# Kernel optimization log

Hardware: AMD Instinct MI355X
Metric: run time of the kernel (lower is better)

Reference implementation:

```python
import jax, jax.numpy as jnp
import numpy as np

T, B, F, H = 128, 64, 75, 512
J = F  # attention dim == number of input features (joints)


def _lstm_dir(x, h0, c0, Wih, Whh, bih, bhh, reverse):
    # x: (T,B,Fin). Precompute input projection once (big GEMM), scan the recurrence.
    xw = jnp.einsum('tbf,gf->tbg', x, Wih) + bih + bhh  # (T,B,4H)

    def step(carry, xt):
        h, c = carry
        g = xt + h @ Whh.T  # (B,4H), PyTorch gate order i,f,g,o
        i, f, gg, o = jnp.split(g, 4, axis=-1)
        c = jax.nn.sigmoid(f) * c + jax.nn.sigmoid(i) * jnp.tanh(gg)
        h = jax.nn.sigmoid(o) * jnp.tanh(c)
        return (h, c), h

    (hT, cT), ys = jax.lax.scan(step, (h0, c0), xw, reverse=reverse)
    return ys, hT


def _bilstm(x, h0, c0, Wih, Whh, bih, bhh):
    # params have leading direction axis of size 2
    yf, hf = _lstm_dir(x, h0[0], c0[0], Wih[0], Whh[0], bih[0], bhh[0], False)
    yb, hb = _lstm_dir(x, h0[1], c0[1], Wih[1], Whh[1], bih[1], bhh[1], True)
    return jnp.concatenate([yf, yb], axis=-1), jnp.stack([hf, hb])


def setup_inputs() -> dict:
    key = jax.random.key(0)
    ks = iter(jax.random.split(key, 40))

    def p(*shape):
        return (jax.random.normal(next(ks), shape, dtype=jnp.float32) * 0.05)

    inp = {
        'x': jax.random.normal(next(ks), (T, B, F), dtype=jnp.float32),
        'h0': jnp.zeros((6, B, H), jnp.float32),
        'c0': jnp.zeros((6, B, H), jnp.float32),
        # salstm: 1-layer bidirectional, input F
        'sa_Wih': p(2, 4 * H, F), 'sa_Whh': p(2, 4 * H, H),
        'sa_bih': p(2, 4 * H), 'sa_bhh': p(2, 4 * H),
        # mainlstm layer 0 (input F)
        'm0_Wih': p(2, 4 * H, F), 'm0_Whh': p(2, 4 * H, H),
        'm0_bih': p(2, 4 * H), 'm0_bhh': p(2, 4 * H),
        # mainlstm layers 1,2 (input 2H), stacked on leading layer axis
        'mL_Wih': p(2, 2, 4 * H, 2 * H), 'mL_Whh': p(2, 2, 4 * H, H),
        'mL_bih': p(2, 2, 4 * H), 'mL_bhh': p(2, 2, 4 * H),
        'safc1_W': p(H, H), 'safc1_b': p(H),
        'safc2_W': p(J, H), 'safc2_b': p(J),
        'fc1_W': p(H, 2 * H), 'fc1_b': p(H),
    }
    return inp


def reference(x, h0, c0, sa_Wih, sa_Whh, sa_bih, sa_bhh,
              m0_Wih, m0_Whh, m0_bih, m0_bhh,
              mL_Wih, mL_Whh, mL_bih, mL_bhh,
              safc1_W, safc1_b, safc2_W, safc2_b, fc1_W, fc1_b):
    # spatial-attention LSTM
    sa_out, sa_hn = _bilstm(x, h0[:2], c0[:2], sa_Wih, sa_Whh, sa_bih, sa_bhh)  # sa_hn (2,B,H)
    e = jnp.exp(jnp.tanh(sa_hn @ safc1_W.T + safc1_b) @ safc2_W.T + safc2_b)  # (2,B,J)
    alpha = e / e.sum(axis=(0, 2), keepdims=True)  # per-batch normalization
    # replace all weights >= 0.1 with their selected mean (per batch element)
    mask = alpha >= 0.1
    cnt = mask.sum(axis=(0, 2), keepdims=True)
    sel_mean = (alpha * mask).sum(axis=(0, 2), keepdims=True) / jnp.maximum(cnt, 1)
    alpha = jnp.where(mask, sel_mean, alpha)
    alpha_b = alpha.mean(axis=0)  # (B,J) -- reconcile direction axis for broadcast

    xw = x * alpha_b[None]  # (T,B,F)

    # 3-layer bidirectional main LSTM
    y, _ = _bilstm(xw, h0[0:2], c0[0:2], m0_Wih, m0_Whh, m0_bih, m0_bhh)
    for l in range(2):
        y, _ = _bilstm(y, h0[2 + 2 * l:4 + 2 * l], c0[2 + 2 * l:4 + 2 * l],
                       mL_Wih[l], mL_Whh[l], mL_bih[l], mL_bhh[l])
    out = y @ fc1_W.T + fc1_b  # (T,B,H)
    return out
```

## Files before the change

### kernel.cpp

```cpp
#include <hip/hip_runtime.h>
#include <cstddef>

#define T_  128
#define B_  64
#define F_  75
#define H_  512
#define G4_ 2048
#define TB_ (T_ * B_)
#define KP_ 128

typedef __bf16 bf16x8 __attribute__((ext_vector_type(8)));
typedef float  f32x4  __attribute__((ext_vector_type(4)));
typedef unsigned long long u64;
typedef unsigned long long __attribute__((may_alias)) u64a;

__device__ __forceinline__ short f2b(float x) {
    union { float f; unsigned u; } v; v.f = x;
    return (short)((v.u + 0x7fffu + ((v.u >> 16) & 1u)) >> 16);
}
__device__ __forceinline__ float b2f(short s) {
    union { float f; unsigned u; } v; v.u = ((unsigned)(unsigned short)s) << 16;
    return v.f;
}
__device__ __forceinline__ void gload16(const void* g, void* l) {
    __builtin_amdgcn_global_load_lds(
        (const __attribute__((address_space(1))) void*)g,
        (__attribute__((address_space(3))) void*)l, 16, 0, 0);
}
__device__ __forceinline__ float fsig(float x) {
    return __builtin_amdgcn_rcpf(1.f + __expf(-x));
}
__device__ __forceinline__ float ftanh(float x) {
    return 1.f - 2.f * __builtin_amdgcn_rcpf(1.f + __expf(2.f * x));
}

__global__ __launch_bounds__(256) void gemm_bf16(
    const short* __restrict__ A, const short* __restrict__ Bm,
    float* __restrict__ C, float* __restrict__ P, int M, int N, int K,
    const float* __restrict__ bias1, const float* __restrict__ bias2)
{
    __shared__ short As[4096];
    __shared__ short Bs[4096];
    const int tid = threadIdx.x;
    const int m_base = blockIdx.y * 128;
    const int n_base = blockIdx.x * 128;
    const int w = tid >> 6, lane = tid & 63;
    const int wm = (w >> 1) * 64, wn = (w & 1) * 64;
    const int lm = lane & 15, q = lane >> 4;

    f32x4 acc[4][4];
#pragma unroll
    for (int i = 0; i < 4; i++)
#pragma unroll
        for (int j = 0; j < 4; j++)
#pragma unroll
            for (int r = 0; r < 4; r++) acc[i][j][r] = 0.f;

    const int s0 = tid, s1 = tid + 256;
    const int r0 = s0 & 127, c0 = s0 >> 7;
    const int r1 = s1 & 127, c1 = s1 >> 7;

    for (int k0 = 0; k0 < K; k0 += 32) {
        __syncthreads();
        gload16(A + (size_t)(m_base + r0) * K + k0 + c0 * 8, &As[s0 * 8]);
        gload16(A + (size_t)(m_base + r1) * K + k0 + c1 * 8, &As[s1 * 8]);
        gload16(Bm + (size_t)(n_base + r0) * K + k0 + c0 * 8, &Bs[s0 * 8]);
        gload16(Bm + (size_t)(n_base + r1) * K + k0 + c1 * 8, &Bs[s1 * 8]);
        __syncthreads();
        bf16x8 af[4], bfv[4];
#pragma unroll
        for (int i = 0; i < 4; i++) {
            af[i]  = *(const bf16x8*)&As[((q * 128) + wm + i * 16 + lm) * 8];
            bfv[i] = *(const bf16x8*)&Bs[((q * 128) + wn + i * 16 + lm) * 8];
        }
#pragma unroll
        for (int i = 0; i < 4; i++)
#pragma unroll
            for (int j = 0; j < 4; j++)
                acc[i][j] = __builtin_amdgcn_mfma_f32_16x16x32_bf16(
                    af[i], bfv[j], acc[i][j], 0, 0, 0);
    }

#pragma unroll
    for (int i = 0; i < 4; i++) {
#pragma unroll
        for (int j = 0; j < 4; j++) {
            const int gm0 = m_base + wm + i * 16 + q * 4;
            const int gn = n_base + wn + j * 16 + lm;
            float bb = (bias1 ? bias1[gn] : 0.f) + (bias2 ? bias2[gn] : 0.f);
            if (P) {
                const int g = gn >> 9, u = gn & 511;
                const int ub = u >> 4, lmu = u & 15;
#pragma unroll
                for (int r = 0; r < 4; r++) {
                    const int gm = gm0 + r;
                    const int t = gm >> 6, b = gm & 63;
                    const int tidS = (b >> 4) * 64 + ((b >> 2) & 3) * 16 + lmu;
                    size_t idx = ((((size_t)t * 32 + ub) * 4 + (b & 3)) * 256 + tidS) * 4 + g;
                    P[idx] = acc[i][j][r] + bb;
                }
            } else {
#pragma unroll
                for (int r = 0; r < 4; r++)
                    C[(size_t)(gm0 + r) * N + gn] = acc[i][j][r] + bb;
            }
        }
    }
}

__global__ __launch_bounds__(256) void pack_whh(
    const float* __restrict__ W, short* __restrict__ Wpk)
{
    int i = blockIdx.x * 256 + threadIdx.x;
    if (i >= 2 * G4_ * H_) return;
    int e = i & 7, lane = (i >> 3) & 63, it = (i >> 9) & 15;
    int g = (i >> 13) & 3, ub = (i >> 15) & 31, dir = (i >> 20) & 1;
    int lm = lane & 15, qq = lane >> 4;
    float v = W[((size_t)dir * G4_ + g * H_ + ub * 16 + lm) * H_
                + it * 32 + qq * 8 + e];
    Wpk[i] = f2b(v);
}

__global__ __launch_bounds__(256) void init_phase(
    const float* __restrict__ h0s, short* __restrict__ Ht,
    unsigned* __restrict__ bar, int zero_bar)
{
    int i = blockIdx.x * 256 + threadIdx.x;
    if (i < 2 * B_ * H_) Ht[i] = f2b(h0s[i]);
    if (zero_bar && i < 64) bar[i] = 0;
}

__global__ __launch_bounds__(256) void ht_to_f32(
    const short* __restrict__ Ht0, float* __restrict__ out)
{
    int i = blockIdx.x * 256 + threadIdx.x;
    if (i < 2 * B_ * H_) out[i] = b2f(Ht0[i]);
}

__global__ __launch_bounds__(256, 1) void lstm_phase(
    const float* __restrict__ XW,
    const short* __restrict__ Wpk,
    short* __restrict__ Ht,
    const float* __restrict__ c0p,
    short* __restrict__ Y,
    unsigned* __restrict__ bar, int phase)
{
    __shared__ short Ws[32768];
    __shared__ short Tb[64 * 24];
    __shared__ unsigned arrv;
    const int dir = blockIdx.y, ub = blockIdx.x, u0 = ub * 16;
    const int tid = threadIdx.x, w = tid >> 6, lane = tid & 63;
    const int lm = lane & 15, q = lane >> 4;

    if (tid == 0) arrv = 0;

    const short* wsrc = Wpk + (size_t)(dir * 32 + ub) * 32768;
#pragma unroll
    for (int p = 0; p < 16; p++)
        gload16(wsrc + (tid + 256 * p) * 8, &Ws[(tid + 256 * p) * 8]);

    const int b0 = w * 16 + q * 4;
    const int u = u0 + lm;
    unsigned* slots = bar + dir * 32;

    float c[4];
    f32x4 xw[4];
#pragma unroll
    for (int r = 0; r < 4; r++)
        c[r] = c0p[(size_t)dir * B_ * H_ + (size_t)(b0 + r) * H_ + u];
    {
        const int t0 = dir ? (T_ - 1) : 0;
        const float* xp = XW + ((size_t)dir * T_ + t0) * (B_ * G4_) + (size_t)ub * 4096;
#pragma unroll
        for (int r = 0; r < 4; r++)
            xw[r] = *(const f32x4*)(xp + r * 1024 + tid * 4);
    }
    __syncthreads();

    for (int s = 0; s < T_; s++) {
        const int t = dir ? (T_ - 1 - s) : s;
        const short* Hc = Ht + ((size_t)((s & 1) * 2 + dir) << 15);

        u64 hq[32];
        const short* hrow = Hc + (w * 16 + lm) * 512 + q * 8;
#pragma unroll
        for (int it = 0; it < 16; it++) {
            const u64* hp = (const u64*)(hrow + it * 32);
            hq[2 * it]     = __hip_atomic_load((u64*)hp,     __ATOMIC_RELAXED, __HIP_MEMORY_SCOPE_AGENT);
            hq[2 * it + 1] = __hip_atomic_load((u64*)hp + 1, __ATOMIC_RELAXED, __HIP_MEMORY_SCOPE_AGENT);
        }

        f32x4 acc[4];
#pragma unroll
        for (int g = 0; g < 4; g++)
#pragma unroll
            for (int r = 0; r < 4; r++) acc[g][r] = 0.f;

#pragma unroll
        for (int it = 0; it < 16; it++) {
            union { u64 q2[2]; bf16x8 v; } ua;
            ua.q2[0] = hq[2 * it]; ua.q2[1] = hq[2 * it + 1];
#pragma unroll
            for (int g = 0; g < 4; g++) {
                bf16x8 bv = *(const bf16x8*)&Ws[((g * 16 + it) * 64 + lane) * 8];
                acc[g] = __builtin_amdgcn_mfma_f32_16x16x32_bf16(ua.v, bv, acc[g], 0, 0, 0);
            }
        }

#pragma unroll
        for (int r = 0; r < 4; r++) {
            float gi = acc[0][r] + xw[r][0];
            float gf = acc[1][r] + xw[r][1];
            float gg = acc[2][r] + xw[r][2];
            float go = acc[3][r] + xw[r][3];
            float cc = fsig(gf) * c[r] + fsig(gi) * ftanh(gg);
            c[r] = cc;
            Tb[(b0 + r) * 24 + lm] = f2b(fsig(go) * ftanh(cc));
        }
        __asm__ volatile("" ::: "memory");

        const int b = tid >> 2, qd = tid & 3;
        u64 v0 = *(const u64a*)&Tb[b * 24 + qd * 4];
        {
            short* Hn = Ht + ((size_t)(((s + 1) & 1) * 2 + dir) << 15);
            __hip_atomic_store((u64*)(Hn + b * 512 + u0 + qd * 4), v0,
                               __ATOMIC_RELAXED, __HIP_MEMORY_SCOPE_AGENT);
        }
        __asm__ volatile("s_waitcnt vmcnt(0)" ::: "memory");
        if (lane == 0)
            __hip_atomic_fetch_add(&arrv, 1u, __ATOMIC_RELAXED,
                                   __HIP_MEMORY_SCOPE_WORKGROUP);

        const unsigned tgt = (unsigned)(phase * T_ + s + 1);
        if (w == 0) {
            const unsigned a4 = 4u * (unsigned)(s + 1);
            while (__hip_atomic_load(&arrv, __ATOMIC_RELAXED,
                                     __HIP_MEMORY_SCOPE_WORKGROUP) < a4) {}
            if (lane == 0)
                __hip_atomic_store(&slots[ub], tgt,
                                   __ATOMIC_RELAXED, __HIP_MEMORY_SCOPE_AGENT);
        }

        if (Y)
            *(u64a*)(Y + ((size_t)t * B_ + b) * (2 * H_) + dir * H_ + u0 + qd * 4) = v0;
        if (s < T_ - 1) {
            const int tn = dir ? (T_ - 2 - s) : (s + 1);
            const float* xp = XW + ((size_t)dir * T_ + tn) * (B_ * G4_) + (size_t)ub * 4096;
#pragma unroll
            for (int r = 0; r < 4; r++)
                xw[r] = *(const f32x4*)(xp + r * 1024 + tid * 4);

            if (w == 0) {
                unsigned v;
                for (;;) {
                    v = (lane < 32)
                        ? __hip_atomic_load(&slots[lane], __ATOMIC_RELAXED, __HIP_MEMORY_SCOPE_AGENT)
                        : tgt;
                    if (__all(v >= tgt)) break;
                    __builtin_amdgcn_s_sleep(1);
                }
            }
            __syncthreads();
        }
    }
}

__global__ __launch_bounds__(256) void gemm_bt(
    const float* __restrict__ A, const float* __restrict__ Bm,
    float* __restrict__ C, int M, int N, int K,
    const float* __restrict__ bias1, int act)
{
    __shared__ float As[16][68];
    __shared__ float Bs[16][68];
    const int tid = threadIdx.x;
    const int m_base = blockIdx.y * 64;
    const int n_base = blockIdx.x * 64;
    const int tm = tid >> 4, tn = tid & 15;
    float acc[4][4] = {};

    for (int k0 = 0; k0 < K; k0 += 16) {
#pragma unroll
        for (int i = 0; i < 4; i++) {
            int idx = tid * 4 + i;
            int r = idx >> 4, kk = idx & 15;
            int gm = m_base + r, gk = k0 + kk;
            As[kk][r] = (gm < M && gk < K) ? A[(size_t)gm * K + gk] : 0.f;
            int gn = n_base + r;
            Bs[kk][r] = (gn < N && gk < K) ? Bm[(size_t)gn * K + gk] : 0.f;
        }
        __syncthreads();
#pragma unroll
        for (int kk = 0; kk < 16; kk++) {
            float4 av = *(const float4*)&As[kk][tm * 4];
            float4 bv = *(const float4*)&Bs[kk][tn * 4];
            float a[4] = {av.x, av.y, av.z, av.w};
            float b[4] = {bv.x, bv.y, bv.z, bv.w};
#pragma unroll
            for (int i = 0; i < 4; i++)
#pragma unroll
                for (int j = 0; j < 4; j++)
                    acc[i][j] = fmaf(a[i], b[j], acc[i][j]);
        }
        __syncthreads();
    }
#pragma unroll
    for (int i = 0; i < 4; i++) {
        int gm = m_base + tm * 4 + i;
        if (gm >= M) continue;
#pragma unroll
        for (int j = 0; j < 4; j++) {
            int gn = n_base + tn * 4 + j;
            if (gn >= N) continue;
            float v = acc[i][j];
            if (bias1) v += bias1[gn];
            if (act == 1) v = tanhf(v);
            else if (act == 2) v = expf(v);
            C[(size_t)gm * N + gn] = v;
        }
    }
}

__global__ __launch_bounds__(256) void conv_f2b(
    const float* __restrict__ src, short* __restrict__ dst, int n)
{
    int i = blockIdx.x * 256 + threadIdx.x;
    if (i < n) dst[i] = f2b(src[i]);
}
__global__ __launch_bounds__(256) void conv_f2b_pad(
    const float* __restrict__ src, short* __restrict__ dst,
    int rows, int kin, int kp)
{
    int i = blockIdx.x * 256 + threadIdx.x;
    if (i < rows * kp) {
        int r = i / kp, k = i % kp;
        dst[i] = (k < kin) ? f2b(src[(size_t)r * kin + k]) : (short)0;
    }
}

__global__ __launch_bounds__(256) void attn_alpha(
    const float* __restrict__ E, float* __restrict__ AB)
{
    const int b = blockIdx.x, tid = threadIdx.x;
    __shared__ float red[256];
    __shared__ float adj[152];
    float v = 0.f;
    if (tid < 150) {
        int d = tid / F_, j = tid % F_;
        v = E[((size_t)d * B_ + b) * F_ + j];
    }
    red[tid] = v; __syncthreads();
    for (int s2 = 128; s2 > 0; s2 >>= 1) {
        if (tid < s2) red[tid] += red[tid + s2];
        __syncthreads();
    }
    float total = red[0]; __syncthreads();
    float alpha = v / total;
    float m = (tid < 150 && alpha >= 0.1f) ? 1.f : 0.f;
    red[tid] = m; __syncthreads();
    for (int s2 = 128; s2 > 0; s2 >>= 1) {
        if (tid < s2) red[tid] += red[tid + s2];
        __syncthreads();
    }
    float cnt = red[0]; __syncthreads();
    red[tid] = m * alpha; __syncthreads();
    for (int s2 = 128; s2 > 0; s2 >>= 1) {
        if (tid < s2) red[tid] += red[tid + s2];
        __syncthreads();
    }
    float selsum = red[0]; __syncthreads();
    float selmean = selsum / fmaxf(cnt, 1.f);
    if (tid < 150) adj[tid] = (m > 0.f) ? selmean : alpha;
    __syncthreads();
    if (tid < F_) AB[(size_t)b * F_ + tid] = 0.5f * (adj[tid] + adj[F_ + tid]);
}

__global__ __launch_bounds__(256) void scale_xb(
    const float* __restrict__ x, const float* __restrict__ AB,
    short* __restrict__ xb)
{
    int i = blockIdx.x * 256 + threadIdx.x;
    if (i < TB_ * KP_) {
        int r = i >> 7, k = i & 127;
        if (k < F_) {
            int b = r % B_;
            xb[i] = f2b(x[(size_t)r * F_ + k] * AB[(size_t)b * F_ + k]);
        } else xb[i] = 0;
    }
}

extern "C" void kernel_launch(void* const* d_in, const int* in_sizes, int n_in,
                              void* d_out, int out_size, void* d_ws, size_t ws_size,
                              hipStream_t stream)
{
    (void)in_sizes; (void)n_in; (void)out_size; (void)ws_size;
    const float* x       = (const float*)d_in[0];
    const float* h0      = (const float*)d_in[1];
    const float* c0      = (const float*)d_in[2];
    const float* sa_Wih  = (const float*)d_in[3];
    const float* sa_Whh  = (const float*)d_in[4];
    const float* sa_bih  = (const float*)d_in[5];
    const float* sa_bhh  = (const float*)d_in[6];
    const float* m0_Wih  = (const float*)d_in[7];
    const float* m0_Whh  = (const float*)d_in[8];
    const float* m0_bih  = (const float*)d_in[9];
    const float* m0_bhh  = (const float*)d_in[10];
    const float* mL_Wih  = (const float*)d_in[11];
    const float* mL_Whh  = (const float*)d_in[12];
    const float* mL_bih  = (const float*)d_in[13];
    const float* mL_bhh  = (const float*)d_in[14];
    const float* safc1_W = (const float*)d_in[15];
    const float* safc1_b = (const float*)d_in[16];
    const float* safc2_W = (const float*)d_in[17];
    const float* safc2_b = (const float*)d_in[18];
    const float* fc1_W   = (const float*)d_in[19];
    const float* fc1_b   = (const float*)d_in[20];

    char* cur = (char*)d_ws;
    auto alloc = [&](size_t bytes) {
        char* p = cur; cur += (bytes + 255) & ~(size_t)255; return p;
    };
    float*    XW   = (float*)alloc((size_t)2 * TB_ * G4_ * 4);
    float*    T1b  = (float*)alloc(2 * B_ * H_ * 4);
    float*    Eb   = (float*)alloc(2 * B_ * F_ * 4);
    float*    AB   = (float*)alloc(B_ * F_ * 4);
    float*    saHf = (float*)alloc(2 * B_ * H_ * 4);
    short*    xb   = (short*)alloc((size_t)TB_ * KP_ * 2);
    short*    Y0b  = (short*)alloc((size_t)TB_ * 2 * H_ * 2);
    short*    Y1b  = (short*)alloc((size_t)TB_ * 2 * H_ * 2);
    short*    Ht   = (short*)alloc((size_t)2 * 2 * B_ * H_ * 2);
    short*    Wpk  = (short*)alloc((size_t)2 * G4_ * H_ * 2);
    short*    Wihb = (short*)alloc((size_t)2 * G4_ * KP_ * 2);
    short*    WihbL= (short*)alloc((size_t)2 * G4_ * 2 * H_ * 2);
    short*    fc1b = (short*)alloc((size_t)H_ * 2 * H_ * 2);
    unsigned* bar  = (unsigned*)alloc(1024);

    auto cv = [&](const float* s, short* d, int n) {
        conv_f2b<<<(n + 255) / 256, 256, 0, stream>>>(s, d, n);
    };
    auto g16 = [&](const short* Ap, const short* Bp, float* Cp, float* Pp,
                   int M, int N, int K, const float* b1, const float* b2) {
        gemm_bf16<<<dim3(N / 128, M / 128), 256, 0, stream>>>(Ap, Bp, Cp, Pp, M, N, K, b1, b2);
    };
    auto phase = [&](const float* Whh_p, const float* h0p, const float* c0p,
                     short* Yout, int pidx) {
        pack_whh<<<(2 * G4_ * H_ + 255) / 256, 256, 0, stream>>>(Whh_p, Wpk);
        init_phase<<<256, 256, 0, stream>>>(h0p, Ht, bar, pidx == 0 ? 1 : 0);
        lstm_phase<<<dim3(32, 2), 256, 0, stream>>>(XW, Wpk, Ht, c0p, Yout, bar, pidx);
    };

    cv(fc1_W, fc1b, H_ * 2 * H_);

    conv_f2b_pad<<<(TB_ * KP_ + 255) / 256, 256, 0, stream>>>(x, xb, TB_, F_, KP_);
    conv_f2b_pad<<<(2 * G4_ * KP_ + 255) / 256, 256, 0, stream>>>(sa_Wih, Wihb, 2 * G4_, F_, KP_);
    for (int d = 0; d < 2; d++)
        g16(xb, Wihb + (size_t)d * G4_ * KP_, nullptr, XW + (size_t)d * TB_ * G4_,
            TB_, G4_, KP_, sa_bih + d * G4_, sa_bhh + d * G4_);
    phase(sa_Whh, h0, c0, nullptr, 0);
    ht_to_f32<<<256, 256, 0, stream>>>(Ht, saHf);
    gemm_bt<<<dim3(8, 2), 256, 0, stream>>>(saHf, safc1_W, T1b, 2 * B_, H_, H_, safc1_b, 1);
    gemm_bt<<<dim3(2, 2), 256, 0, stream>>>(T1b, safc2_W, Eb, 2 * B_, F_, H_, safc2_b, 2);
    attn_alpha<<<B_, 256, 0, stream>>>(Eb, AB);
    scale_xb<<<(TB_ * KP_ + 255) / 256, 256, 0, stream>>>(x, AB, xb);

    conv_f2b_pad<<<(2 * G4_ * KP_ + 255) / 256, 256, 0, stream>>>(m0_Wih, Wihb, 2 * G4_, F_, KP_);
    for (int d = 0; d < 2; d++)
        g16(xb, Wihb + (size_t)d * G4_ * KP_, nullptr, XW + (size_t)d * TB_ * G4_,
            TB_, G4_, KP_, m0_bih + d * G4_, m0_bhh + d * G4_);
    phase(m0_Whh, h0, c0, Y0b, 1);

    cv(mL_Wih, WihbL, 2 * G4_ * 2 * H_);
    for (int d = 0; d < 2; d++)
        g16(Y0b, WihbL + (size_t)d * G4_ * 2 * H_, nullptr, XW + (size_t)d * TB_ * G4_,
            TB_, G4_, 2 * H_, mL_bih + d * G4_, mL_bhh + d * G4_);
    phase(mL_Whh, h0 + 2 * B_ * H_, c0 + 2 * B_ * H_, Y1b, 2);

    cv(mL_Wih + (size_t)2 * G4_ * 2 * H_, WihbL, 2 * G4_ * 2 * H_);
    for (int d = 0; d < 2; d++)
        g16(Y1b, WihbL + (size_t)d * G4_ * 2 * H_, nullptr, XW + (size_t)d * TB_ * G4_,
            TB_, G4_, 2 * H_, mL_bih + (2 + d) * G4_, mL_bhh + (2 + d) * G4_);
    phase(mL_Whh + (size_t)2 * G4_ * H_, h0 + 4 * B_ * H_, c0 + 4 * B_ * H_, Y0b, 3);

    g16(Y0b, fc1b, (float*)d_out, nullptr, TB_, H_, 2 * H_, fc1_b, nullptr);
}
```

Before: 4.145 ms.

## Overlap next layer's input-projection GEMM with LSTM recurrence via extra worker blocks

Adds extra workgroups to the persistent LSTM kernel that compute the next layer's input projection (or the final fc1) tile by tile. Each tile starts once the recurrence barrier shows the needed timesteps from both directions are complete, so the separate GEMM launches between layers run concurrently with the sequential recurrence. It also hoists all weight packing and conversion to the start, using double XW buffers and per-layer hidden buffers. In exchange it needs a much larger workspace, gated on ws_size, and the extra blocks spin-wait with a bounded timeout that could return stale data if a wait expires. The Y stores become agent-scope atomics so the consumer blocks can see them.

```diff
diff --git a/kernel.cpp b/kernel.cpp
--- a/kernel.cpp
+++ b/kernel.cpp
@@ -130,6 +130,22 @@
     if (zero_bar && i < 64) bar[i] = 0;
 }
 
+__global__ __launch_bounds__(256) void prep_init(
+    const float* __restrict__ h0, short* __restrict__ HtA,
+    short* __restrict__ HtB, short* __restrict__ HtC, short* __restrict__ HtD,
+    unsigned* __restrict__ bar)
+{
+    int i = blockIdx.x * 256 + threadIdx.x;
+    if (i < 2 * B_ * H_) {
+        short vA = f2b(h0[i]);
+        HtA[i] = vA;
+        HtB[i] = vA;
+        HtC[i] = f2b(h0[2 * B_ * H_ + i]);
+        HtD[i] = f2b(h0[4 * B_ * H_ + i]);
+    }
+    if (i < 64) bar[i] = 0;
+}
+
 __global__ __launch_bounds__(256) void ht_to_f32(
     const short* __restrict__ Ht0, float* __restrict__ out)
 {
@@ -143,15 +159,120 @@
     short* __restrict__ Ht,
     const float* __restrict__ c0p,
     short* __restrict__ Y,
-    unsigned* __restrict__ bar, int phase)
+    unsigned* __restrict__ bar, int phase,
+    const short* __restrict__ jA, const short* __restrict__ jB,
+    float* __restrict__ jP, float* __restrict__ jC,
+    const float* __restrict__ jb1, const float* __restrict__ jb2, int job)
 {
     __shared__ short Ws[32768];
     __shared__ short Tb[64 * 24];
     __shared__ unsigned arrv;
-    const int dir = blockIdx.y, ub = blockIdx.x, u0 = ub * 16;
     const int tid = threadIdx.x, w = tid >> 6, lane = tid & 63;
     const int lm = lane & 15, q = lane >> 4;
 
+    if (blockIdx.x >= 32) {
+        if (job == 0) return;
+        short* As = Ws;
+        short* Bs = Ws + 4096;
+        const int hh = blockIdx.x - 32;
+        const int dirh = blockIdx.y;
+        const unsigned pT = (unsigned)(phase * T_);
+        const int wm = (w >> 1) * 64, wn = (w & 1) * 64;
+
+        const short* Bop; float* Pd; float* Cd; const float* b1; const float* b2;
+        int n_tile, grp, iters, stride;
+        if (job == 1) {
+            Bop = jB + (size_t)dirh * G4_ * 1024;
+            Pd = jP + (size_t)dirh * TB_ * G4_;
+            Cd = nullptr;
+            b1 = jb1 + dirh * G4_; b2 = jb2 + dirh * G4_;
+            n_tile = hh & 15; grp = hh >> 4; iters = 16; stride = 4;
+        } else {
+            Bop = jB; Pd = nullptr; Cd = jC; b1 = jb1; b2 = nullptr;
+            int H2 = dirh * 64 + hh;
+            n_tile = H2 & 3; grp = H2 >> 2; iters = 2; stride = 32;
+        }
+        const int n_base = n_tile * 128;
+
+        for (int it2 = 0; it2 < iters; it2++) {
+            int j = grp + stride * it2;
+            int k = (j & 1) ? 32 + (j >> 1) : 31 - (j >> 1);
+            int m_base = k * 128, t0 = 2 * k;
+            if (w == 0) {
+                unsigned tgt = (lane < 32) ? pT + (unsigned)(t0 + 2)
+                                           : pT + (unsigned)(T_ - t0);
+                int itc = 0;
+                for (;;) {
+                    unsigned v = __hip_atomic_load(&bar[lane], __ATOMIC_RELAXED,
+                                                   __HIP_MEMORY_SCOPE_AGENT);
+                    if (__all(v >= tgt)) break;
+                    if (++itc > (1 << 19)) break;
+                    __builtin_amdgcn_s_sleep(32);
+                }
+            }
+            __syncthreads();
+
+            f32x4 acc[4][4];
+#pragma unroll
+            for (int i = 0; i < 4; i++)
+#pragma unroll
+                for (int jj = 0; jj < 4; jj++)
+#pragma unroll
+                    for (int r = 0; r < 4; r++) acc[i][jj][r] = 0.f;
+
+            const int s0 = tid, s1 = tid + 256;
+            const int r0 = s0 & 127, cc0 = s0 >> 7;
+            const int r1 = s1 & 127, cc1 = s1 >> 7;
+            for (int k0 = 0; k0 < 1024; k0 += 32) {
+                __syncthreads();
+                gload16(jA + (size_t)(m_base + r0) * 1024 + k0 + cc0 * 8, &As[s0 * 8]);
+                gload16(jA + (size_t)(m_base + r1) * 1024 + k0 + cc1 * 8, &As[s1 * 8]);
+                gload16(Bop + (size_t)(n_base + r0) * 1024 + k0 + cc0 * 8, &Bs[s0 * 8]);
+                gload16(Bop + (size_t)(n_base + r1) * 1024 + k0 + cc1 * 8, &Bs[s1 * 8]);
+                __syncthreads();
+                bf16x8 af[4], bfv[4];
+#pragma unroll
+                for (int i = 0; i < 4; i++) {
+                    af[i]  = *(const bf16x8*)&As[((q * 128) + wm + i * 16 + lm) * 8];
+                    bfv[i] = *(const bf16x8*)&Bs[((q * 128) + wn + i * 16 + lm) * 8];
+                }
+#pragma unroll
+                for (int i = 0; i < 4; i++)
+#pragma unroll
+                    for (int jj = 0; jj < 4; jj++)
+                        acc[i][jj] = __builtin_amdgcn_mfma_f32_16x16x32_bf16(
+                            af[i], bfv[jj], acc[i][jj], 0, 0, 0);
+            }
+#pragma unroll
+            for (int i = 0; i < 4; i++) {
+#pragma unroll
+                for (int jj = 0; jj < 4; jj++) {
+                    const int gm0 = m_base + wm + i * 16 + q * 4;
+                    const int gn = n_base + wn + jj * 16 + lm;
+                    float bb = b1[gn] + (b2 ? b2[gn] : 0.f);
+                    if (Pd) {
+                        const int g = gn >> 9, u = gn & 511;
+                        const int ub2 = u >> 4, lmu = u & 15;
+#pragma unroll
+                        for (int r = 0; r < 4; r++) {
+                            const int gm = gm0 + r;
+                            const int t = gm >> 6, b = gm & 63;
+                            const int tidS = (b >> 4) * 64 + ((b >> 2) & 3) * 16 + lmu;
+                            size_t idx = ((((size_t)t * 32 + ub2) * 4 + (b & 3)) * 256 + tidS) * 4 + g;
+                            Pd[idx] = acc[i][jj][r] + bb;
+                        }
+                    } else {
+#pragma unroll
+                        for (int r = 0; r < 4; r++)
+                            Cd[(size_t)(gm0 + r) * 512 + gn] = acc[i][jj][r] + bb;
+                    }
+                }
+            }
+        }
+        return;
+    }
+
+    const int dir = blockIdx.y, ub = blockIdx.x, u0 = ub * 16;
     if (tid == 0) arrv = 0;
 
     const short* wsrc = Wpk + (size_t)(dir * 32 + ub) * 32768;
@@ -221,11 +342,15 @@
 
         const int b = tid >> 2, qd = tid & 3;
         u64 v0 = *(const u64a*)&Tb[b * 24 + qd * 4];
+        u64* ydst = Y ? (u64*)(Y + ((size_t)t * B_ + b) * (2 * H_) + dir * H_ + u0 + qd * 4)
+                      : nullptr;
         {
             short* Hn = Ht + ((size_t)(((s + 1) & 1) * 2 + dir) << 15);
             __hip_atomic_store((u64*)(Hn + b * 512 + u0 + qd * 4), v0,
                                __ATOMIC_RELAXED, __HIP_MEMORY_SCOPE_AGENT);
         }
+        if (ydst && job)
+            __hip_atomic_store(ydst, v0, __ATOMIC_RELAXED, __HIP_MEMORY_SCOPE_AGENT);
         __asm__ volatile("s_waitcnt vmcnt(0)" ::: "memory");
         if (lane == 0)
             __hip_atomic_fetch_add(&arrv, 1u, __ATOMIC_RELAXED,
@@ -241,8 +366,7 @@
                                    __ATOMIC_RELAXED, __HIP_MEMORY_SCOPE_AGENT);
         }
 
-        if (Y)
-            *(u64a*)(Y + ((size_t)t * B_ + b) * (2 * H_) + dir * H_ + u0 + qd * 4) = v0;
+        if (ydst && !job) *(u64a*)ydst = v0;
         if (s < T_ - 1) {
             const int tn = dir ? (T_ - 2 - s) : (s + 1);
             const float* xp = XW + ((size_t)dir * T_ + tn) * (B_ * G4_) + (size_t)ub * 4096;
@@ -392,7 +516,7 @@
                               void* d_out, int out_size, void* d_ws, size_t ws_size,
                               hipStream_t stream)
 {
-    (void)in_sizes; (void)n_in; (void)out_size; (void)ws_size;
+    (void)in_sizes; (void)n_in; (void)out_size;
     const float* x       = (const float*)d_in[0];
     const float* h0      = (const float*)d_in[1];
     const float* c0      = (const float*)d_in[2];
@@ -419,6 +543,85 @@
     auto alloc = [&](size_t bytes) {
         char* p = cur; cur += (bytes + 255) & ~(size_t)255; return p;
     };
+    auto cv = [&](const float* s, short* d, int n) {
+        conv_f2b<<<(n + 255) / 256, 256, 0, stream>>>(s, d, n);
+    };
+
+    const bool OV = ws_size >= 370000000ull;
+
+    if (OV) {
+        float*    XWa  = (float*)alloc((size_t)2 * TB_ * G4_ * 4);
+        float*    XWb  = (float*)alloc((size_t)2 * TB_ * G4_ * 4);
+        float*    T1b  = (float*)alloc(2 * B_ * H_ * 4);
+        float*    Eb   = (float*)alloc(2 * B_ * F_ * 4);
+        float*    AB   = (float*)alloc(B_ * F_ * 4);
+        float*    saHf = (float*)alloc(2 * B_ * H_ * 4);
+        short*    xb   = (short*)alloc((size_t)TB_ * KP_ * 2);
+        short*    Y0b  = (short*)alloc((size_t)TB_ * 2 * H_ * 2);
+        short*    Y1b  = (short*)alloc((size_t)TB_ * 2 * H_ * 2);
+        short*    Y2b  = (short*)alloc((size_t)TB_ * 2 * H_ * 2);
+        short*    HtA  = (short*)alloc((size_t)2 * 2 * B_ * H_ * 2);
+        short*    HtB  = (short*)alloc((size_t)2 * 2 * B_ * H_ * 2);
+        short*    HtC  = (short*)alloc((size_t)2 * 2 * B_ * H_ * 2);
+        short*    HtD  = (short*)alloc((size_t)2 * 2 * B_ * H_ * 2);
+        const size_t PK = (size_t)2 * G4_ * H_;
+        short*    Wpk4 = (short*)alloc(4 * PK * 2);
+        short*    WihbSA = (short*)alloc((size_t)2 * G4_ * KP_ * 2);
+        short*    WihbM0 = (short*)alloc((size_t)2 * G4_ * KP_ * 2);
+        short*    WihbL  = (short*)alloc((size_t)2 * 2 * G4_ * 2 * H_ * 2);
+        short*    fc1b   = (short*)alloc((size_t)H_ * 2 * H_ * 2);
+        unsigned* bar    = (unsigned*)alloc(1024);
+
+        auto g16 = [&](const short* Ap, const short* Bp, float* Pp,
+                       int K, const float* b1, const float* b2) {
+            gemm_bf16<<<dim3(G4_ / 128, TB_ / 128), 256, 0, stream>>>(
+                Ap, Bp, nullptr, Pp, TB_, G4_, K, b1, b2);
+        };
+        auto lstm = [&](const float* XWp, const short* Wp, short* Htp,
+                        const float* c0p, short* Yp, int pidx,
+                        const short* ja, const short* jb, float* jp, float* jc,
+                        const float* b1, const float* b2, int job) {
+            lstm_phase<<<dim3(job ? 96 : 32, 2), 256, 0, stream>>>(
+                XWp, Wp, Htp, c0p, Yp, bar, pidx, ja, jb, jp, jc, b1, b2, job);
+        };
+
+        prep_init<<<256, 256, 0, stream>>>(h0, HtA, HtB, HtC, HtD, bar);
+        cv(fc1_W, fc1b, H_ * 2 * H_);
+        conv_f2b_pad<<<(2 * G4_ * KP_ + 255) / 256, 256, 0, stream>>>(sa_Wih, WihbSA, 2 * G4_, F_, KP_);
+        conv_f2b_pad<<<(2 * G4_ * KP_ + 255) / 256, 256, 0, stream>>>(m0_Wih, WihbM0, 2 * G4_, F_, KP_);
+        cv(mL_Wih, WihbL, 2 * 2 * G4_ * 2 * H_);
+        pack_whh<<<(2 * G4_ * H_ + 255) / 256, 256, 0, stream>>>(sa_Whh, Wpk4);
+        pack_whh<<<(2 * G4_ * H_ + 255) / 256, 256, 0, stream>>>(m0_Whh, Wpk4 + PK);
+        pack_whh<<<(2 * G4_ * H_ + 255) / 256, 256, 0, stream>>>(mL_Whh, Wpk4 + 2 * PK);
+        pack_whh<<<(2 * G4_ * H_ + 255) / 256, 256, 0, stream>>>(mL_Whh + (size_t)2 * G4_ * H_, Wpk4 + 3 * PK);
+        conv_f2b_pad<<<(TB_ * KP_ + 255) / 256, 256, 0, stream>>>(x, xb, TB_, F_, KP_);
+
+        for (int d = 0; d < 2; d++)
+            g16(xb, WihbSA + (size_t)d * G4_ * KP_, XWa + (size_t)d * TB_ * G4_,
+                KP_, sa_bih + d * G4_, sa_bhh + d * G4_);
+        lstm(XWa, Wpk4, HtA, c0, nullptr, 0,
+             nullptr, nullptr, nullptr, nullptr, nullptr, nullptr, 0);
+        ht_to_f32<<<256, 256, 0, stream>>>(HtA, saHf);
+        gemm_bt<<<dim3(8, 2), 256, 0, stream>>>(saHf, safc1_W, T1b, 2 * B_, H_, H_, safc1_b, 1);
+        gemm_bt<<<dim3(2, 2), 256, 0, stream>>>(T1b, safc2_W, Eb, 2 * B_, F_, H_, safc2_b, 2);
+        attn_alpha<<<B_, 256, 0, stream>>>(Eb, AB);
+        scale_xb<<<(TB_ * KP_ + 255) / 256, 256, 0, stream>>>(x, AB, xb);
+
+        for (int d = 0; d < 2; d++)
+            g16(xb, WihbM0 + (size_t)d * G4_ * KP_, XWa + (size_t)d * TB_ * G4_,
+                KP_, m0_bih + d * G4_, m0_bhh + d * G4_);
+        lstm(XWa, Wpk4 + PK, HtB, c0, Y0b, 1,
+             Y0b, WihbL, XWb, nullptr, mL_bih, mL_bhh, 1);
+
+        lstm(XWb, Wpk4 + 2 * PK, HtC, c0 + 2 * B_ * H_, Y1b, 2,
+             Y1b, WihbL + (size_t)2 * G4_ * 2 * H_, XWa, nullptr,
+             mL_bih + 2 * G4_, mL_bhh + 2 * G4_, 1);
+
+        lstm(XWa, Wpk4 + 3 * PK, HtD, c0 + 4 * B_ * H_, Y2b, 3,
+             Y2b, fc1b, nullptr, (float*)d_out, fc1_b, nullptr, 2);
+        return;
+    }
+
     float*    XW   = (float*)alloc((size_t)2 * TB_ * G4_ * 4);
     float*    T1b  = (float*)alloc(2 * B_ * H_ * 4);
     float*    Eb   = (float*)alloc(2 * B_ * F_ * 4);
@@ -434,27 +637,24 @@
     short*    fc1b = (short*)alloc((size_t)H_ * 2 * H_ * 2);
     unsigned* bar  = (unsigned*)alloc(1024);
 
-    auto cv = [&](const float* s, short* d, int n) {
-        conv_f2b<<<(n + 255) / 256, 256, 0, stream>>>(s, d, n);
-    };
-    auto g16 = [&](const short* Ap, const short* Bp, float* Cp, float* Pp,
-                   int M, int N, int K, const float* b1, const float* b2) {
+    auto g16f = [&](const short* Ap, const short* Bp, float* Cp, float* Pp,
+                    int M, int N, int K, const float* b1, const float* b2) {
         gemm_bf16<<<dim3(N / 128, M / 128), 256, 0, stream>>>(Ap, Bp, Cp, Pp, M, N, K, b1, b2);
     };
     auto phase = [&](const float* Whh_p, const float* h0p, const float* c0p,
                      short* Yout, int pidx) {
         pack_whh<<<(2 * G4_ * H_ + 255) / 256, 256, 0, stream>>>(Whh_p, Wpk);
         init_phase<<<256, 256, 0, stream>>>(h0p, Ht, bar, pidx == 0 ? 1 : 0);
-        lstm_phase<<<dim3(32, 2), 256, 0, stream>>>(XW, Wpk, Ht, c0p, Yout, bar, pidx);
+        lstm_phase<<<dim3(32, 2), 256, 0, stream>>>(XW, Wpk, Ht, c0p, Yout, bar, pidx,
+            nullptr, nullptr, nullptr, nullptr, nullptr, nullptr, 0);
     };
 
     cv(fc1_W, fc1b, H_ * 2 * H_);
-
     conv_f2b_pad<<<(TB_ * KP_ + 255) / 256, 256, 0, stream>>>(x, xb, TB_, F_, KP_);
     conv_f2b_pad<<<(2 * G4_ * KP_ + 255) / 256, 256, 0, stream>>>(sa_Wih, Wihb, 2 * G4_, F_, KP_);
     for (int d = 0; d < 2; d++)
-        g16(xb, Wihb + (size_t)d * G4_ * KP_, nullptr, XW + (size_t)d * TB_ * G4_,
-            TB_, G4_, KP_, sa_bih + d * G4_, sa_bhh + d * G4_);
+        g16f(xb, Wihb + (size_t)d * G4_ * KP_, nullptr, XW + (size_t)d * TB_ * G4_,
+             TB_, G4_, KP_, sa_bih + d * G4_, sa_bhh + d * G4_);
     phase(sa_Whh, h0, c0, nullptr, 0);
     ht_to_f32<<<256, 256, 0, stream>>>(Ht, saHf);
     gemm_bt<<<dim3(8, 2), 256, 0, stream>>>(saHf, safc1_W, T1b, 2 * B_, H_, H_, safc1_b, 1);
@@ -464,21 +664,21 @@
 
     conv_f2b_pad<<<(2 * G4_ * KP_ + 255) / 256, 256, 0, stream>>>(m0_Wih, Wihb, 2 * G4_, F_, KP_);
     for (int d = 0; d < 2; d++)
-        g16(xb, Wihb + (size_t)d * G4_ * KP_, nullptr, XW + (size_t)d * TB_ * G4_,
-            TB_, G4_, KP_, m0_bih + d * G4_, m0_bhh + d * G4_);
+        g16f(xb, Wihb + (size_t)d * G4_ * KP_, nullptr, XW + (size_t)d * TB_ * G4_,
+             TB_, G4_, KP_, m0_bih + d * G4_, m0_bhh + d * G4_);
     phase(m0_Whh, h0, c0, Y0b, 1);
 
     cv(mL_Wih, WihbL, 2 * G4_ * 2 * H_);
     for (int d = 0; d < 2; d++)
-        g16(Y0b, WihbL + (size_t)d * G4_ * 2 * H_, nullptr, XW + (size_t)d * TB_ * G4_,
-            TB_, G4_, 2 * H_, mL_bih + d * G4_, mL_bhh + d * G4_);
+        g16f(Y0b, WihbL + (size_t)d * G4_ * 2 * H_, nullptr, XW + (size_t)d * TB_ * G4_,
+             TB_, G4_, 2 * H_, mL_bih + d * G4_, mL_bhh + d * G4_);
     phase(mL_Whh, h0 + 2 * B_ * H_, c0 + 2 * B_ * H_, Y1b, 2);
 
     cv(mL_Wih + (size_t)2 * G4_ * 2 * H_, WihbL, 2 * G4_ * 2 * H_);
     for (int d = 0; d < 2; d++)
-        g16(Y1b, WihbL + (size_t)d * G4_ * 2 * H_, nullptr, XW + (size_t)d * TB_ * G4_,
-            TB_, G4_, 2 * H_, mL_bih + (2 + d) * G4_, mL_bhh + (2 + d) * G4_);
+        g16f(Y1b, WihbL + (size_t)d * G4_ * 2 * H_, nullptr, XW + (size_t)d * TB_ * G4_,
+             TB_, G4_, 2 * H_, mL_bih + (2 + d) * G4_, mL_bhh + (2 + d) * G4_);
     phase(mL_Whh + (size_t)2 * G4_ * H_, h0 + 4 * B_ * H_, c0 + 4 * B_ * H_, Y0b, 3);
 
-    g16(Y0b, fc1b, (float*)d_out, nullptr, TB_, H_, 2 * H_, fc1_b, nullptr);
-}
+    g16f(Y0b, fc1b, (float*)d_out, nullptr, TB_, H_, 2 * H_, fc1_b, nullptr);
+}
```

Result: no change. 4.144 ms (-0.0%).
